# Performance work log

Hardware: AMD Instinct MI355X
Metric: run time of the kernel (lower is better)

## Reference

```python
import jax, jax.numpy as jnp
import numpy as np

NUM_NODES = 4096
IN_DIM = 16
HIDDEN = 64
OUT_DIM = 32
HEADS = 4
NEG_SLOPE = 0.2
NEG_INF = -1e9


def _glorot(key, shape):
    fan_in, fan_out = shape[0], shape[-1]
    lim = jnp.sqrt(6.0 / (fan_in + fan_out))
    return jax.random.uniform(key, shape, jnp.float32, -lim, lim)


def setup_inputs() -> dict:
    key = jax.random.key(0)
    ks = jax.random.split(key, 8)
    B = 2
    return {
        "x": jax.random.normal(ks[0], (B, NUM_NODES, IN_DIM), jnp.float32),
        "embedding": _glorot(ks[1], (NUM_NODES, HIDDEN)),
        "W_proj": _glorot(ks[2], (IN_DIM, HIDDEN)),
        "b_proj": jnp.zeros((HIDDEN,), jnp.float32),
        "W1": _glorot(ks[3], (HIDDEN, HIDDEN)),  # heads=4, 16 per head, concat -> 64
        "att1_src": _glorot(ks[4], (HEADS, HIDDEN // HEADS)),
        "att1_dst": _glorot(ks[5], (HEADS, HIDDEN // HEADS)),
        "b1": jnp.zeros((HIDDEN,), jnp.float32),
        "W2": _glorot(ks[6], (HIDDEN, OUT_DIM)),  # heads=4, 8 per head, concat -> 32
        "att2_src": _glorot(ks[7], (HEADS, OUT_DIM // HEADS)),
        "att2_dst": _glorot(jax.random.fold_in(key, 99), (HEADS, OUT_DIM // HEADS)),
        "b2": jnp.zeros((OUT_DIM,), jnp.float32),
    }


def _gat(x, mask, W, a_src, a_dst, b):
    """Dense masked GAT layer. x: [B,N,Fin], mask: [N,N] bool (shared over batch).

    Equivalent to GATConv over edge list tf.where(adj > 0.5): for each target i,
    softmax over neighbors j of LeakyReLU(a_dst.Wh_i + a_src.Wh_j), aggregate Wh_j.
    """
    B, N, _ = x.shape
    H, F = a_src.shape
    h = (x @ W).reshape(B, N, H, F)                       # [B,N,H,F]
    s_src = jnp.einsum('bnhf,hf->bnh', h, a_src)          # per-source score
    s_dst = jnp.einsum('bnhf,hf->bnh', h, a_dst)          # per-target score
    e = s_dst[:, :, None, :] + s_src[:, None, :, :]       # [B,i,j,H]
    e = jnp.where(e > 0, e, NEG_SLOPE * e)                # LeakyReLU(0.2)
    e = jnp.where(mask[None, :, :, None], e, NEG_INF)
    alpha = jax.nn.softmax(e, axis=2)                     # softmax over neighbors j
    out = jnp.einsum('bijh,bjhf->bihf', alpha, h).reshape(B, N, H * F)
    return out + b


def reference(x, embedding, W_proj, b_proj, W1, att1_src, att1_dst, b1,
              W2, att2_src, att2_dst, b2):
    # AdaptiveAdjacency: cosine similarity of l2-normalized node embeddings
    ne = embedding / jnp.linalg.norm(embedding, axis=-1, keepdims=True)
    adj = ne @ ne.T                                       # [N,N], same for all batch
    mask = adj > 0.5                                      # edge set (incl. self-loops)

    h = x @ W_proj + b_proj                               # Dense proj -> hidden
    h = jax.nn.relu(_gat(h, mask, W1, att1_src, att1_dst, b1))
    return _gat(h, mask, W2, att2_src, att2_dst, b2)
```

## Files before the change

### kernel.cpp

```cpp
#include <hip/hip_runtime.h>
#include <hip/hip_bf16.h>
#include <stdint.h>

#define N_NODES 4096
#define BATCH 2

typedef __attribute__((ext_vector_type(8))) short short8v;
typedef __attribute__((ext_vector_type(4))) float f32x4;

static __device__ inline float bf2f(unsigned short b) {
    return __uint_as_float(((unsigned)b) << 16);
}
static __device__ inline float rl(float v, int k) {
    return __uint_as_float(__builtin_amdgcn_readlane(__float_as_uint(v), k));
}

static __device__ inline void cvt2(float f0, float f1, unsigned* hi, unsigned* lo) {
    float2 p;
    p.x = f0;
    p.y = f1;
    __hip_bfloat162 h = __float22bfloat162_rn(p);
    unsigned hb;
    __builtin_memcpy(&hb, &h, 4);
    p.x = f0 - bf2f((unsigned short)hb);
    p.y = f1 - bf2f((unsigned short)(hb >> 16));
    __hip_bfloat162 l2v = __float22bfloat162_rn(p);
    unsigned lb;
    __builtin_memcpy(&lb, &l2v, 4);
    *hi = hb;
    *lo = lb;
}

__global__ __launch_bounds__(256) void k2_kernel(
        const float* __restrict__ emb, unsigned long long* __restrict__ mask,
        const float* __restrict__ x, const float* __restrict__ Wp,
        const float* __restrict__ bp, const float* __restrict__ W1,
        const float* __restrict__ a1s, const float* __restrict__ a1d,
        float* __restrict__ h1out, float* __restrict__ ssrc, float* __restrict__ sdst) {
    __shared__ unsigned short Ah[128 * 64];
    __shared__ unsigned short Al[128 * 64];
    __shared__ unsigned short Bh[128 * 64];
    __shared__ unsigned short Bl[128 * 64];
    __shared__ float An[128];
    __shared__ float Bn[128];
    int t = threadIdx.x;
    int w = t >> 6, l = t & 63;

    if (blockIdx.x < 256) {
        int b = blockIdx.x;
        int row0 = b * 32 + w * 8;

        float xv[8];
#pragma unroll
        for (int r = 0; r < 8; ++r) xv[r] = x[(size_t)(row0 + r) * 16 + (l & 15)];

        float h0[8];
        float bpv = bp[l];
#pragma unroll
        for (int r = 0; r < 8; ++r) h0[r] = bpv;
#pragma unroll
        for (int k = 0; k < 16; ++k) {
            float wk = Wp[k * 64 + l];
#pragma unroll
            for (int r = 0; r < 8; ++r) h0[r] += rl(xv[r], k) * wk;
        }

        float h1[8] = {0.f, 0.f, 0.f, 0.f, 0.f, 0.f, 0.f, 0.f};
#pragma unroll
        for (int k = 0; k < 64; ++k) {
            float wk = W1[k * 64 + l];
#pragma unroll
            for (int r = 0; r < 8; ++r) h1[r] += rl(h0[r], k) * wk;
        }

        float as_ = a1s[l], ad_ = a1d[l];
#pragma unroll
        for (int r = 0; r < 8; ++r) {
            h1out[(size_t)(row0 + r) * 64 + l] = h1[r];
            float ps = h1[r] * as_, pd = h1[r] * ad_;
#pragma unroll
            for (int m = 8; m >= 1; m >>= 1) {
                ps += __shfl_xor(ps, m);
                pd += __shfl_xor(pd, m);
            }
            if ((l & 15) == 0) {
                ssrc[(size_t)(row0 + r) * 4 + (l >> 4)] = ps;
                sdst[(size_t)(row0 + r) * 4 + (l >> 4)] = pd;
            }
        }
        return;
    }

    int tile = blockIdx.x - 256;
    int bi = tile >> 5, bj = tile & 31;
    int i0 = bi * 128, j0 = bj * 128;

    {
        int rhalf = l >> 1, half = l & 1;
        int row = w * 32 + rhalf;
        float na = 0.f, nb = 0.f;
#pragma unroll
        for (int q = 0; q < 4; ++q) {
            int slot = half * 4 + q;
            const float* pa = &emb[(size_t)(i0 + row) * 64 + slot * 8];
            const float* pb = &emb[(size_t)(j0 + row) * 64 + slot * 8];
            float4 a0 = *(const float4*)pa;
            float4 a1 = *(const float4*)(pa + 4);
            float4 b0 = *(const float4*)pb;
            float4 b1 = *(const float4*)(pb + 4);
            na += a0.x * a0.x + a0.y * a0.y + a0.z * a0.z + a0.w * a0.w +
                  a1.x * a1.x + a1.y * a1.y + a1.z * a1.z + a1.w * a1.w;
            nb += b0.x * b0.x + b0.y * b0.y + b0.z * b0.z + b0.w * b0.w +
                  b1.x * b1.x + b1.y * b1.y + b1.z * b1.z + b1.w * b1.w;

            union {
                unsigned u[4];
                short8v v;
            } HA, LA, HB, LB;
            cvt2(a0.x, a0.y, &HA.u[0], &LA.u[0]);
            cvt2(a0.z, a0.w, &HA.u[1], &LA.u[1]);
            cvt2(a1.x, a1.y, &HA.u[2], &LA.u[2]);
            cvt2(a1.z, a1.w, &HA.u[3], &LA.u[3]);
            cvt2(b0.x, b0.y, &HB.u[0], &LB.u[0]);
            cvt2(b0.z, b0.w, &HB.u[1], &LB.u[1]);
            cvt2(b1.x, b1.y, &HB.u[2], &LB.u[2]);
            cvt2(b1.z, b1.w, &HB.u[3], &LB.u[3]);

            int ss = ((slot ^ (row & 7)) << 3);
            *(short8v*)&Ah[row * 64 + ss] = HA.v;
            *(short8v*)&Al[row * 64 + ss] = LA.v;
            *(short8v*)&Bh[row * 64 + ss] = HB.v;
            *(short8v*)&Bl[row * 64 + ss] = LB.v;
        }
        na += __shfl_xor(na, 1);
        nb += __shfl_xor(nb, 1);
        if (half == 0) {
            An[row] = sqrtf(na);
            Bn[row] = sqrtf(nb);
        }
    }
    __syncthreads();

    int fr = l & 15;
    int s0 = l >> 4;
    int r7 = l & 7;
    short8v aH[2][2], aL[2][2];
#pragma unroll
    for (int rt = 0; rt < 2; ++rt) {
        int base = (w * 32 + rt * 16 + fr) * 64;
        aH[rt][0] = *(const short8v*)&Ah[base + ((s0 ^ r7) << 3)];
        aH[rt][1] = *(const short8v*)&Ah[base + (((s0 + 4) ^ r7) << 3)];
        aL[rt][0] = *(const short8v*)&Al[base + ((s0 ^ r7) << 3)];
        aL[rt][1] = *(const short8v*)&Al[base + (((s0 + 4) ^ r7) << 3)];
    }

    f32x4 acc[2][8];
#pragma unroll
    for (int rt = 0; rt < 2; ++rt)
#pragma unroll
        for (int js = 0; js < 8; ++js) acc[rt][js] = (f32x4){0.f, 0.f, 0.f, 0.f};

#pragma unroll
    for (int js = 0; js < 8; ++js) {
        int bbase = (js * 16 + fr) * 64;
        short8v bH0 = *(const short8v*)&Bh[bbase + ((s0 ^ r7) << 3)];
        short8v bH1 = *(const short8v*)&Bh[bbase + (((s0 + 4) ^ r7) << 3)];
        short8v bL0 = *(const short8v*)&Bl[bbase + ((s0 ^ r7) << 3)];
        short8v bL1 = *(const short8v*)&Bl[bbase + (((s0 + 4) ^ r7) << 3)];
#pragma unroll
        for (int rt = 0; rt < 2; ++rt) {
            f32x4 a = acc[rt][js];
            a = __builtin_amdgcn_mfma_f32_16x16x32_bf16(aH[rt][0], bH0, a, 0, 0, 0);
            a = __builtin_amdgcn_mfma_f32_16x16x32_bf16(aH[rt][1], bH1, a, 0, 0, 0);
            a = __builtin_amdgcn_mfma_f32_16x16x32_bf16(aH[rt][0], bL0, a, 0, 0, 0);
            a = __builtin_amdgcn_mfma_f32_16x16x32_bf16(aH[rt][1], bL1, a, 0, 0, 0);
            a = __builtin_amdgcn_mfma_f32_16x16x32_bf16(aL[rt][0], bH0, a, 0, 0, 0);
            a = __builtin_amdgcn_mfma_f32_16x16x32_bf16(aL[rt][1], bH1, a, 0, 0, 0);
            acc[rt][js] = a;
        }
    }

    int shift = ((l & 15) >> 2) * 16;
    int r = l & 3;
#pragma unroll
    for (int rt = 0; rt < 2; ++rt) {
        int rb = w * 32 + rt * 16 + (l >> 4) * 4;
        float n0 = 0.5f * An[rb + 0];
        float n1 = 0.5f * An[rb + 1];
        float n2 = 0.5f * An[rb + 2];
        float n3 = 0.5f * An[rb + 3];
#pragma unroll
        for (int ws_ = 0; ws_ < 2; ++ws_) {
            unsigned long long w64 = 0;
#pragma unroll
            for (int js2 = 0; js2 < 4; ++js2) {
                int js = ws_ * 4 + js2;
                float nbv = Bn[js * 16 + (l & 15)];
                f32x4 a = acc[rt][js];
                unsigned long long c0 = __ballot(a[0] > n0 * nbv);
                unsigned long long c1 = __ballot(a[1] > n1 * nbv);
                unsigned long long c2 = __ballot(a[2] > n2 * nbv);
                unsigned long long c3 = __ballot(a[3] > n3 * nbv);
                unsigned long long sel = r == 0 ? c0 : r == 1 ? c1 : r == 2 ? c2 : c3;
                w64 |= ((sel >> shift) & 0xFFFFULL) << (js2 * 16);
            }
            if (l < 16)
                mask[(size_t)(i0 + w * 32 + rt * 16 + l) * 64 + bj * 2 + ws_] = w64;
        }
    }
}

__global__ __launch_bounds__(256) void agg1_fused_kernel(
        const float* __restrict__ h1, const float* __restrict__ ssrc,
        const float* __restrict__ sdst, const unsigned long long* __restrict__ mask,
        const float* __restrict__ b1, const float* __restrict__ W2,
        const float* __restrict__ a2s, const float* __restrict__ a2d,
        float* __restrict__ h2out, float* __restrict__ s2s, float* __restrict__ s2d) {
    int i = blockIdx.x * 4 + (threadIdx.x >> 6);
    int t = threadIdx.x & 63;
    int hh = t >> 4;

    float sdA = sdst[(size_t)i * 4 + hh];
    float sdB = sdst[(size_t)(i + N_NODES) * 4 + hh];
    unsigned long long myword = mask[(size_t)i * 64 + t];

    float mA = -1e30f, dA = 0.f, aA = 0.f;
    float mB = -1e30f, dB = 0.f, aB = 0.f;
    unsigned long long nz = __ballot(myword != 0ULL);
    while (nz) {
        int lw = __ffsll(nz) - 1;
        nz &= nz - 1;
        unsigned long long wbits = __shfl(myword, lw);
        while (wbits) {
            int bpos = __ffsll(wbits) - 1;
            wbits &= wbits - 1;
            int j = (lw << 6) + bpos;
            float ssA = ssrc[(size_t)j * 4 + hh];
            float ssB = ssrc[(size_t)(j + N_NODES) * 4 + hh];
            float hvA = h1[(size_t)j * 64 + t];
            float hvB = h1[(size_t)(j + N_NODES) * 64 + t];
            float e = sdA + ssA;
            e = e > 0.f ? e : 0.2f * e;
            float mn = fmaxf(mA, e);
            float cf = __expf(mA - mn);
            float wg = __expf(e - mn);
            dA = dA * cf + wg;
            aA = aA * cf + wg * hvA;
            mA = mn;
            e = sdB + ssB;
            e = e > 0.f ? e : 0.2f * e;
            mn = fmaxf(mB, e);
            cf = __expf(mB - mn);
            wg = __expf(e - mn);
            dB = dB * cf + wg;
            aB = aB * cf + wg * hvB;
            mB = mn;
        }
    }
    float b1v = b1[t];
    float oA = fmaxf(aA / dA + b1v, 0.f);
    float oB = fmaxf(aB / dB + b1v, 0.f);

    int l2 = t & 31;
    float acc2A = 0.f, acc2B = 0.f;
#pragma unroll
    for (int k = 0; k < 64; ++k) {
        float wk = W2[k * 32 + l2];
        acc2A += rl(oA, k) * wk;
        acc2B += rl(oB, k) * wk;
    }

    float a2sv = a2s[l2], a2dv = a2d[l2];
    float psA = acc2A * a2sv, pdA = acc2A * a2dv;
    float psB = acc2B * a2sv, pdB = acc2B * a2dv;
#pragma unroll
    for (int mm = 4; mm >= 1; mm >>= 1) {
        psA += __shfl_xor(psA, mm);
        pdA += __shfl_xor(pdA, mm);
        psB += __shfl_xor(psB, mm);
        pdB += __shfl_xor(pdB, mm);
    }
    if (t < 32) {
        h2out[(size_t)i * 32 + t] = acc2A;
        h2out[(size_t)(i + N_NODES) * 32 + t] = acc2B;
        if ((t & 7) == 0) {
            s2s[(size_t)i * 4 + (t >> 3)] = psA;
            s2d[(size_t)i * 4 + (t >> 3)] = pdA;
            s2s[(size_t)(i + N_NODES) * 4 + (t >> 3)] = psB;
            s2d[(size_t)(i + N_NODES) * 4 + (t >> 3)] = pdB;
        }
    }
}

__global__ __launch_bounds__(256) void agg2_kernel(
        const float* __restrict__ hfeat, const float* __restrict__ ssrc,
        const float* __restrict__ sdst, const unsigned long long* __restrict__ mask,
        const float* __restrict__ bias, float* __restrict__ out) {
    int i = blockIdx.x * 4 + (threadIdx.x >> 6);
    int t = threadIdx.x & 63;
    int tt = t & 31;
    int hh = tt >> 3;

    float sdA = sdst[(size_t)i * 4 + hh];
    float sdB = sdst[(size_t)(i + N_NODES) * 4 + hh];
    unsigned long long myword = mask[(size_t)i * 64 + t];

    float mA = -1e30f, dA = 0.f, aA = 0.f;
    float mB = -1e30f, dB = 0.f, aB = 0.f;
    unsigned long long nz = __ballot(myword != 0ULL);
    while (nz) {
        int lw = __ffsll(nz) - 1;
        nz &= nz - 1;
        unsigned long long wbits = __shfl(myword, lw);
        while (wbits) {
            int bpos = __ffsll(wbits) - 1;
            wbits &= wbits - 1;
            int j = (lw << 6) + bpos;
            float ssA = ssrc[(size_t)j * 4 + hh];
            float ssB = ssrc[(size_t)(j + N_NODES) * 4 + hh];
            float hvA = hfeat[(size_t)j * 32 + tt];
            float hvB = hfeat[(size_t)(j + N_NODES) * 32 + tt];
            float e = sdA + ssA;
            e = e > 0.f ? e : 0.2f * e;
            float mn = fmaxf(mA, e);
            float cf = __expf(mA - mn);
            float wg = __expf(e - mn);
            dA = dA * cf + wg;
            aA = aA * cf + wg * hvA;
            mA = mn;
            e = sdB + ssB;
            e = e > 0.f ? e : 0.2f * e;
            mn = fmaxf(mB, e);
            cf = __expf(mB - mn);
            wg = __expf(e - mn);
            dB = dB * cf + wg;
            aB = aB * cf + wg * hvB;
            mB = mn;
        }
    }
    float bv = bias[tt];
    if (t < 32) {
        out[(size_t)i * 32 + tt] = aA / dA + bv;
        out[(size_t)(i + N_NODES) * 32 + tt] = aB / dB + bv;
    }
}

extern "C" void kernel_launch(void* const* d_in, const int* in_sizes, int n_in,
                              void* d_out, int out_size, void* d_ws, size_t ws_size,
                              hipStream_t stream) {
    const float* x   = (const float*)d_in[0];
    const float* emb = (const float*)d_in[1];
    const float* Wp  = (const float*)d_in[2];
    const float* bp  = (const float*)d_in[3];
    const float* W1  = (const float*)d_in[4];
    const float* a1s = (const float*)d_in[5];
    const float* a1d = (const float*)d_in[6];
    const float* b1  = (const float*)d_in[7];
    const float* W2  = (const float*)d_in[8];
    const float* a2s = (const float*)d_in[9];
    const float* a2d = (const float*)d_in[10];
    const float* b2  = (const float*)d_in[11];

    const int ROWS = BATCH * N_NODES;

    char* w = (char*)d_ws;
    unsigned long long* mask = (unsigned long long*)w; w += (size_t)N_NODES * 64 * 8;
    float* h1  = (float*)w;                      w += (size_t)ROWS * 64 * 4;
    float* s1s = (float*)w;                      w += (size_t)ROWS * 4 * 4;
    float* s1d = (float*)w;                      w += (size_t)ROWS * 4 * 4;
    float* h2  = (float*)w;                      w += (size_t)ROWS * 32 * 4;
    float* s2s = (float*)w;                      w += (size_t)ROWS * 4 * 4;
    float* s2d = (float*)w;                      w += (size_t)ROWS * 4 * 4;

    k2_kernel<<<dim3(1280), dim3(256), 0, stream>>>(
        emb, mask, x, Wp, bp, W1, a1s, a1d, h1, s1s, s1d);
    agg1_fused_kernel<<<dim3(N_NODES / 4), dim3(256), 0, stream>>>(
        h1, s1s, s1d, mask, b1, W2, a2s, a2d, h2, s2s, s2d);
    agg2_kernel<<<dim3(N_NODES / 4), dim3(256), 0, stream>>>(
        h2, s2s, s2d, mask, b2, (float*)d_out);
}
```

Before: 33.69 us.

## Reuse staged column tile across four row tiles per block in mask kernel

Each similarity-mask block now stages the column (j) embedding tile into shared memory once and loops over four row (i) tiles, restaging only the row tile each iteration. This cuts redundant global loads and bf16 hi/lo splitting of the j tile, and shrinks the grid from 1280 to 512 blocks. The trade-off is fewer concurrent blocks and serialized per-block work with extra barriers, which may reduce latency hiding.

```diff
diff --git a/kernel.cpp b/kernel.cpp
--- a/kernel.cpp
+++ b/kernel.cpp
@@ -31,6 +31,36 @@
     *lo = lb;
 }
 
+static __device__ inline void stage_one(const float* __restrict__ emb, int g0,
+                                        unsigned short* H, unsigned short* L,
+                                        float* Nrm, int w, int l) {
+    int rhalf = l >> 1, half = l & 1;
+    int row = w * 32 + rhalf;
+    float n = 0.f;
+#pragma unroll
+    for (int q = 0; q < 4; ++q) {
+        int slot = half * 4 + q;
+        const float* pa = &emb[(size_t)(g0 + row) * 64 + slot * 8];
+        float4 a0 = *(const float4*)pa;
+        float4 a1 = *(const float4*)(pa + 4);
+        n += a0.x * a0.x + a0.y * a0.y + a0.z * a0.z + a0.w * a0.w +
+             a1.x * a1.x + a1.y * a1.y + a1.z * a1.z + a1.w * a1.w;
+        union {
+            unsigned u[4];
+            short8v v;
+        } HH, LL;
+        cvt2(a0.x, a0.y, &HH.u[0], &LL.u[0]);
+        cvt2(a0.z, a0.w, &HH.u[1], &LL.u[1]);
+        cvt2(a1.x, a1.y, &HH.u[2], &LL.u[2]);
+        cvt2(a1.z, a1.w, &HH.u[3], &LL.u[3]);
+        int ss = ((slot ^ (row & 7)) << 3);
+        *(short8v*)&H[row * 64 + ss] = HH.v;
+        *(short8v*)&L[row * 64 + ss] = LL.v;
+    }
+    n += __shfl_xor(n, 1);
+    if (half == 0) Nrm[row] = sqrtf(n);
+}
+
 __global__ __launch_bounds__(256) void k2_kernel(
         const float* __restrict__ emb, unsigned long long* __restrict__ mask,
         const float* __restrict__ x, const float* __restrict__ Wp,
@@ -91,122 +121,88 @@
         return;
     }
 
-    int tile = blockIdx.x - 256;
-    int bi = tile >> 5, bj = tile & 31;
-    int i0 = bi * 128, j0 = bj * 128;
-
-    {
-        int rhalf = l >> 1, half = l & 1;
-        int row = w * 32 + rhalf;
-        float na = 0.f, nb = 0.f;
-#pragma unroll
-        for (int q = 0; q < 4; ++q) {
-            int slot = half * 4 + q;
-            const float* pa = &emb[(size_t)(i0 + row) * 64 + slot * 8];
-            const float* pb = &emb[(size_t)(j0 + row) * 64 + slot * 8];
-            float4 a0 = *(const float4*)pa;
-            float4 a1 = *(const float4*)(pa + 4);
-            float4 b0 = *(const float4*)pb;
-            float4 b1 = *(const float4*)(pb + 4);
-            na += a0.x * a0.x + a0.y * a0.y + a0.z * a0.z + a0.w * a0.w +
-                  a1.x * a1.x + a1.y * a1.y + a1.z * a1.z + a1.w * a1.w;
-            nb += b0.x * b0.x + b0.y * b0.y + b0.z * b0.z + b0.w * b0.w +
-                  b1.x * b1.x + b1.y * b1.y + b1.z * b1.z + b1.w * b1.w;
-
-            union {
-                unsigned u[4];
-                short8v v;
-            } HA, LA, HB, LB;
-            cvt2(a0.x, a0.y, &HA.u[0], &LA.u[0]);
-            cvt2(a0.z, a0.w, &HA.u[1], &LA.u[1]);
-            cvt2(a1.x, a1.y, &HA.u[2], &LA.u[2]);
-            cvt2(a1.z, a1.w, &HA.u[3], &LA.u[3]);
-            cvt2(b0.x, b0.y, &HB.u[0], &LB.u[0]);
-            cvt2(b0.z, b0.w, &HB.u[1], &LB.u[1]);
-            cvt2(b1.x, b1.y, &HB.u[2], &LB.u[2]);
-            cvt2(b1.z, b1.w, &HB.u[3], &LB.u[3]);
-
-            int ss = ((slot ^ (row & 7)) << 3);
-            *(short8v*)&Ah[row * 64 + ss] = HA.v;
-            *(short8v*)&Al[row * 64 + ss] = LA.v;
-            *(short8v*)&Bh[row * 64 + ss] = HB.v;
-            *(short8v*)&Bl[row * 64 + ss] = LB.v;
-        }
-        na += __shfl_xor(na, 1);
-        nb += __shfl_xor(nb, 1);
-        if (half == 0) {
-            An[row] = sqrtf(na);
-            Bn[row] = sqrtf(nb);
-        }
-    }
-    __syncthreads();
+    int tile4 = blockIdx.x - 256;
+    int bi4 = tile4 >> 5;
+    int bj = tile4 & 31;
+    int j0 = bj * 128;
+
+    stage_one(emb, j0, Bh, Bl, Bn, w, l);
 
     int fr = l & 15;
     int s0 = l >> 4;
     int r7 = l & 7;
-    short8v aH[2][2], aL[2][2];
-#pragma unroll
-    for (int rt = 0; rt < 2; ++rt) {
-        int base = (w * 32 + rt * 16 + fr) * 64;
-        aH[rt][0] = *(const short8v*)&Ah[base + ((s0 ^ r7) << 3)];
-        aH[rt][1] = *(const short8v*)&Ah[base + (((s0 + 4) ^ r7) << 3)];
-        aL[rt][0] = *(const short8v*)&Al[base + ((s0 ^ r7) << 3)];
-        aL[rt][1] = *(const short8v*)&Al[base + (((s0 + 4) ^ r7) << 3)];
-    }
-
-    f32x4 acc[2][8];
-#pragma unroll
-    for (int rt = 0; rt < 2; ++rt)
-#pragma unroll
-        for (int js = 0; js < 8; ++js) acc[rt][js] = (f32x4){0.f, 0.f, 0.f, 0.f};
-
-#pragma unroll
-    for (int js = 0; js < 8; ++js) {
-        int bbase = (js * 16 + fr) * 64;
-        short8v bH0 = *(const short8v*)&Bh[bbase + ((s0 ^ r7) << 3)];
-        short8v bH1 = *(const short8v*)&Bh[bbase + (((s0 + 4) ^ r7) << 3)];
-        short8v bL0 = *(const short8v*)&Bl[bbase + ((s0 ^ r7) << 3)];
-        short8v bL1 = *(const short8v*)&Bl[bbase + (((s0 + 4) ^ r7) << 3)];
-#pragma unroll
-        for (int rt = 0; rt < 2; ++rt) {
-            f32x4 a = acc[rt][js];
-            a = __builtin_amdgcn_mfma_f32_16x16x32_bf16(aH[rt][0], bH0, a, 0, 0, 0);
-            a = __builtin_amdgcn_mfma_f32_16x16x32_bf16(aH[rt][1], bH1, a, 0, 0, 0);
-            a = __builtin_amdgcn_mfma_f32_16x16x32_bf16(aH[rt][0], bL0, a, 0, 0, 0);
-            a = __builtin_amdgcn_mfma_f32_16x16x32_bf16(aH[rt][1], bL1, a, 0, 0, 0);
-            a = __builtin_amdgcn_mfma_f32_16x16x32_bf16(aL[rt][0], bH0, a, 0, 0, 0);
-            a = __builtin_amdgcn_mfma_f32_16x16x32_bf16(aL[rt][1], bH1, a, 0, 0, 0);
-            acc[rt][js] = a;
-        }
-    }
-
     int shift = ((l & 15) >> 2) * 16;
     int r = l & 3;
-#pragma unroll
-    for (int rt = 0; rt < 2; ++rt) {
-        int rb = w * 32 + rt * 16 + (l >> 4) * 4;
-        float n0 = 0.5f * An[rb + 0];
-        float n1 = 0.5f * An[rb + 1];
-        float n2 = 0.5f * An[rb + 2];
-        float n3 = 0.5f * An[rb + 3];
-#pragma unroll
-        for (int ws_ = 0; ws_ < 2; ++ws_) {
-            unsigned long long w64 = 0;
-#pragma unroll
-            for (int js2 = 0; js2 < 4; ++js2) {
-                int js = ws_ * 4 + js2;
-                float nbv = Bn[js * 16 + (l & 15)];
+
+#pragma unroll 1
+    for (int p = 0; p < 4; ++p) {
+        int i0 = (bi4 * 4 + p) * 128;
+        stage_one(emb, i0, Ah, Al, An, w, l);
+        __syncthreads();
+
+        short8v aH[2][2], aL[2][2];
+#pragma unroll
+        for (int rt = 0; rt < 2; ++rt) {
+            int base = (w * 32 + rt * 16 + fr) * 64;
+            aH[rt][0] = *(const short8v*)&Ah[base + ((s0 ^ r7) << 3)];
+            aH[rt][1] = *(const short8v*)&Ah[base + (((s0 + 4) ^ r7) << 3)];
+            aL[rt][0] = *(const short8v*)&Al[base + ((s0 ^ r7) << 3)];
+            aL[rt][1] = *(const short8v*)&Al[base + (((s0 + 4) ^ r7) << 3)];
+        }
+
+        f32x4 acc[2][8];
+#pragma unroll
+        for (int rt = 0; rt < 2; ++rt)
+#pragma unroll
+            for (int js = 0; js < 8; ++js) acc[rt][js] = (f32x4){0.f, 0.f, 0.f, 0.f};
+
+#pragma unroll
+        for (int js = 0; js < 8; ++js) {
+            int bbase = (js * 16 + fr) * 64;
+            short8v bH0 = *(const short8v*)&Bh[bbase + ((s0 ^ r7) << 3)];
+            short8v bH1 = *(const short8v*)&Bh[bbase + (((s0 + 4) ^ r7) << 3)];
+            short8v bL0 = *(const short8v*)&Bl[bbase + ((s0 ^ r7) << 3)];
+            short8v bL1 = *(const short8v*)&Bl[bbase + (((s0 + 4) ^ r7) << 3)];
+#pragma unroll
+            for (int rt = 0; rt < 2; ++rt) {
                 f32x4 a = acc[rt][js];
-                unsigned long long c0 = __ballot(a[0] > n0 * nbv);
-                unsigned long long c1 = __ballot(a[1] > n1 * nbv);
-                unsigned long long c2 = __ballot(a[2] > n2 * nbv);
-                unsigned long long c3 = __ballot(a[3] > n3 * nbv);
-                unsigned long long sel = r == 0 ? c0 : r == 1 ? c1 : r == 2 ? c2 : c3;
-                w64 |= ((sel >> shift) & 0xFFFFULL) << (js2 * 16);
+                a = __builtin_amdgcn_mfma_f32_16x16x32_bf16(aH[rt][0], bH0, a, 0, 0, 0);
+                a = __builtin_amdgcn_mfma_f32_16x16x32_bf16(aH[rt][1], bH1, a, 0, 0, 0);
+                a = __builtin_amdgcn_mfma_f32_16x16x32_bf16(aH[rt][0], bL0, a, 0, 0, 0);
+                a = __builtin_amdgcn_mfma_f32_16x16x32_bf16(aH[rt][1], bL1, a, 0, 0, 0);
+                a = __builtin_amdgcn_mfma_f32_16x16x32_bf16(aL[rt][0], bH0, a, 0, 0, 0);
+                a = __builtin_amdgcn_mfma_f32_16x16x32_bf16(aL[rt][1], bH1, a, 0, 0, 0);
+                acc[rt][js] = a;
             }
-            if (l < 16)
-                mask[(size_t)(i0 + w * 32 + rt * 16 + l) * 64 + bj * 2 + ws_] = w64;
-        }
+        }
+
+#pragma unroll
+        for (int rt = 0; rt < 2; ++rt) {
+            int rb = w * 32 + rt * 16 + (l >> 4) * 4;
+            float n0 = 0.5f * An[rb + 0];
+            float n1 = 0.5f * An[rb + 1];
+            float n2 = 0.5f * An[rb + 2];
+            float n3 = 0.5f * An[rb + 3];
+#pragma unroll
+            for (int ws_ = 0; ws_ < 2; ++ws_) {
+                unsigned long long w64 = 0;
+#pragma unroll
+                for (int js2 = 0; js2 < 4; ++js2) {
+                    int js = ws_ * 4 + js2;
+                    float nbv = Bn[js * 16 + (l & 15)];
+                    f32x4 a = acc[rt][js];
+                    unsigned long long c0 = __ballot(a[0] > n0 * nbv);
+                    unsigned long long c1 = __ballot(a[1] > n1 * nbv);
+                    unsigned long long c2 = __ballot(a[2] > n2 * nbv);
+                    unsigned long long c3 = __ballot(a[3] > n3 * nbv);
+                    unsigned long long sel = r == 0 ? c0 : r == 1 ? c1 : r == 2 ? c2 : c3;
+                    w64 |= ((sel >> shift) & 0xFFFFULL) << (js2 * 16);
+                }
+                if (l < 16)
+                    mask[(size_t)(i0 + w * 32 + rt * 16 + l) * 64 + bj * 2 + ws_] = w64;
+            }
+        }
+        __syncthreads();
     }
 }
 
@@ -372,7 +368,7 @@
     float* s2s = (float*)w;                      w += (size_t)ROWS * 4 * 4;
     float* s2d = (float*)w;                      w += (size_t)ROWS * 4 * 4;
 
-    k2_kernel<<<dim3(1280), dim3(256), 0, stream>>>(
+    k2_kernel<<<dim3(512), dim3(256), 0, stream>>>(
         emb, mask, x, Wp, bp, W1, a1s, a1d, h1, s1s, s1d);
     agg1_fused_kernel<<<dim3(N_NODES / 4), dim3(256), 0, stream>>>(
         h1, s1s, s1d, mask, b1, W2, a2s, a2d, h2, s2s, s2d);
```

Result: no change. 33.10 us (-1.8%).
